# Optimization experiments

Measured on AMD Instinct MI355X. Metric: run time of the kernel, lower is better.

## Reference

```python
import jax, jax.numpy as jnp
import numpy as np

N_NODES = 100000
N_EDGES = 3200000
N_FEAT = 256
N_CLASS = 4


def setup_inputs() -> dict:
    key = jax.random.key(0)
    ks = jax.random.split(key, 8)
    x = jax.random.normal(ks[0], (N_NODES, N_FEAT), dtype=jnp.float32)
    edge_index = jax.random.randint(ks[1], (2, N_EDGES), 0, N_NODES, dtype=jnp.int64)
    def xavier(k, shape):
        fan_in, fan_out = shape
        std = np.sqrt(2.0 / (fan_in + fan_out))
        return jax.random.normal(k, shape, dtype=jnp.float32) * std
    return {
        'x': x,
        'edge_index': edge_index,
        'W_gcn': xavier(ks[2], (N_FEAT, 64)),
        'b_gcn': jnp.zeros((64,), jnp.float32),
        'W1': xavier(ks[3], (64, 32)),
        'b1': jnp.zeros((32,), jnp.float32),
        'W2': xavier(ks[4], (32, 16)),
        'b2': jnp.zeros((16,), jnp.float32),
        'W3': xavier(ks[5], (16, N_CLASS)),
        'b3': jnp.zeros((N_CLASS,), jnp.float32),
    }


def gcn_conv(x, edge_index, W, b):
    # PyG GCNConv: transform, add self-loops, symmetric normalization, scatter-add
    N = x.shape[0]
    h = x @ W  # [N, 64]
    loop = jnp.arange(N, dtype=edge_index.dtype)
    src = jnp.concatenate([edge_index[0], loop])
    dst = jnp.concatenate([edge_index[1], loop])
    deg = jax.ops.segment_sum(jnp.ones_like(dst, dtype=h.dtype), dst, num_segments=N)
    dinv = jnp.where(deg > 0, jax.lax.rsqrt(deg), 0.0)
    norm = dinv[src] * dinv[dst]  # [E+N]
    msgs = h[src] * norm[:, None]  # gather [E+N, 64]
    out = jax.ops.segment_sum(msgs, dst, num_segments=N)
    return out + b


def reference(x, edge_index, W_gcn, b_gcn, W1, b1, W2, b2, W3, b3):
    h = gcn_conv(x, edge_index, W_gcn, b_gcn)
    h = jax.nn.relu(h)          # dropout is identity in eval mode
    h = jax.nn.relu(h @ W1 + b1)
    h = jax.nn.relu(h @ W2 + b2)
    h = h @ W3 + b3
    return jax.nn.log_softmax(h, axis=1)
```

## Files before the change

### kernel.cpp

```cpp
#include <hip/hip_runtime.h>
#include <hip/hip_bf16.h>

#define NN 100000
#define NE 3200000
#define NPB 64
#define NB 1564
#define CAP 2560
#define BATCH 8192
#define NGB 1563

typedef __hip_bfloat16 bf16;
typedef __attribute__((ext_vector_type(8))) short bf16x8;
typedef __attribute__((ext_vector_type(4))) float f32x4;

__device__ __forceinline__ void fma4(float4& a, float s, const float4 w) {
  a.x = fmaf(s, w.x, a.x);
  a.y = fmaf(s, w.y, a.y);
  a.z = fmaf(s, w.z, a.z);
  a.w = fmaf(s, w.w, a.w);
}

__device__ __forceinline__ unsigned short f2b(float f) {
  unsigned u = __float_as_uint(f);
  unsigned r = ((u >> 16) & 1u) + 0x7FFFu;
  return (unsigned short)((u + r) >> 16);
}

__device__ __forceinline__ unsigned pack2(float lo, float hi) {
  return (unsigned)f2b(lo) | ((unsigned)f2b(hi) << 16);
}

__global__ void detect_k(const int* __restrict__ e, int* __restrict__ flag) {
  unsigned long long b = __ballot(e[2 * (int)threadIdx.x + 1] == 0);
  if (threadIdx.x == 0) flag[0] = (b == 0xFFFFFFFFFFFFFFFFULL) ? 1 : 0;
}

__global__ __launch_bounds__(1024) void bin_k(const void* __restrict__ eidx,
                                              const int* __restrict__ flag,
                                              int* __restrict__ bcur,
                                              int* __restrict__ buckets) {
  __shared__ int scnt[NB];
  __shared__ int lcur[NB];
  int t = threadIdx.x;
  long long e0 = (long long)blockIdx.x * BATCH;
  int m = (int)((NE - e0 < BATCH) ? (NE - e0) : BATCH);
  int isI64 = flag[0];

  for (int i = t; i < NB; i += 1024) scnt[i] = 0;
  __syncthreads();

  int ent[BATCH / 1024], bv[BATCH / 1024];
#pragma unroll
  for (int j = 0; j < BATCH / 1024; j++) {
    int idx = t + j * 1024;
    bv[j] = -1;
    if (idx < m) {
      long long i = e0 + idx;
      int s, d;
      if (isI64) {
        s = (int)((const long long*)eidx)[i];
        d = (int)((const long long*)eidx)[NE + i];
      } else {
        s = ((const int*)eidx)[i];
        d = ((const int*)eidx)[NE + i];
      }
      bv[j] = d >> 6;
      ent[j] = s | ((d & 63) << 17);
      atomicAdd(&scnt[bv[j]], 1);
    }
  }
  __syncthreads();
  for (int i = t; i < NB; i += 1024) {
    int c = scnt[i];
    lcur[i] = c ? atomicAdd(&bcur[i], c) : 0;
  }
  __syncthreads();
#pragma unroll
  for (int j = 0; j < BATCH / 1024; j++) {
    if (bv[j] >= 0) {
      int pos = atomicAdd(&lcur[bv[j]], 1);
      if (pos < CAP) buckets[(size_t)bv[j] * CAP + pos] = ent[j];
    }
  }
}

__global__ __launch_bounds__(256) void cnt_k(const int* __restrict__ buckets,
                                             const int* __restrict__ bcur,
                                             float* __restrict__ dinv) {
  __shared__ int cnt[NPB];
  int b = blockIdx.x, t = threadIdx.x;
  if (t < NPB) cnt[t] = 0;
  __syncthreads();
  int m = bcur[b]; if (m > CAP) m = CAP;
  const int* bp = buckets + (size_t)b * CAP;
  for (int i = t; i < m; i += 256) atomicAdd(&cnt[(bp[i] >> 17) & 63], 1);
  __syncthreads();
  int node = b * NPB + t;
  if (t < NPB && node < NN) dinv[node] = rsqrtf((float)cnt[t] + 1.0f);
}

__global__ __launch_bounds__(256) void prep_k(const float* __restrict__ W,
                                              unsigned short* __restrict__ wh,
                                              unsigned short* __restrict__ wl) {
  int t = threadIdx.x;
#pragma unroll 4
  for (int i = 0; i < 64; i++) {
    int idx = i * 256 + t;
    int j = idx & 7;
    int lane = (idx >> 3) & 63;
    int pair = idx >> 9;
    int nf = pair & 3, kk = pair >> 2;
    int k = kk * 32 + (lane >> 4) * 8 + j;
    int n = nf * 16 + (lane & 15);
    float w = W[k * 64 + n];
    unsigned short hh = f2b(w);
    float fh = __uint_as_float((unsigned)hh << 16);
    wh[idx] = hh;
    wl[idx] = f2b(w - fh);
  }
}

__global__ __launch_bounds__(256) void gemm_k(const float* __restrict__ x,
                                              const unsigned short* __restrict__ wh,
                                              const unsigned short* __restrict__ wl,
                                              bf16* __restrict__ h) {
  int t = threadIdx.x;
  int wv = t >> 6, l = t & 63;
  int rowbase = blockIdx.x * 64 + wv * 16;
  int arow = rowbase + (l & 15);
  if (arow >= NN) arow = NN - 1;
  const float* xrow = x + (size_t)arow * 256 + (l >> 4) * 8;

  const bf16x8* whf = (const bf16x8*)wh;
  const bf16x8* wlf = (const bf16x8*)wl;

  f32x4 acc0 = {0.f, 0.f, 0.f, 0.f};
  f32x4 acc1 = acc0, acc2 = acc0, acc3 = acc0;

  float4 x0a = *(const float4*)(xrow +   0), x0b = *(const float4*)(xrow +   4);
  float4 x1a = *(const float4*)(xrow +  32), x1b = *(const float4*)(xrow +  36);
  float4 x2a = *(const float4*)(xrow +  64), x2b = *(const float4*)(xrow +  68);
  float4 x3a = *(const float4*)(xrow +  96), x3b = *(const float4*)(xrow + 100);
  float4 x4a = *(const float4*)(xrow + 128), x4b = *(const float4*)(xrow + 132);
  float4 x5a = *(const float4*)(xrow + 160), x5b = *(const float4*)(xrow + 164);
  float4 x6a = *(const float4*)(xrow + 192), x6b = *(const float4*)(xrow + 196);
  float4 x7a = *(const float4*)(xrow + 224), x7b = *(const float4*)(xrow + 228);

  bf16x8 ha0, ha1, ha2, ha3, la0, la1, la2, la3;
  bf16x8 hb0, hb1, hb2, hb3, lb0, lb1, lb2, lb3;

#define LOADW(H0, H1, H2, H3, L0, L1, L2, L3, kk)                      \
  {                                                                    \
    int fb_ = (kk) * 256 + l;                                          \
    H0 = whf[fb_]; H1 = whf[fb_ + 64]; H2 = whf[fb_ + 128]; H3 = whf[fb_ + 192]; \
    L0 = wlf[fb_]; L1 = wlf[fb_ + 64]; L2 = wlf[fb_ + 128]; L3 = wlf[fb_ + 192]; \
  }
#define COMPUTE(Xa, Xb, H0, H1, H2, H3, L0, L1, L2, L3)                \
  {                                                                    \
    bf16x8 ah, al;                                                     \
    {                                                                  \
      unsigned short hh_; float fh_;                                   \
      hh_ = f2b(Xa.x); fh_ = __uint_as_float((unsigned)hh_ << 16); ah[0] = (short)hh_; al[0] = (short)f2b(Xa.x - fh_); \
      hh_ = f2b(Xa.y); fh_ = __uint_as_float((unsigned)hh_ << 16); ah[1] = (short)hh_; al[1] = (short)f2b(Xa.y - fh_); \
      hh_ = f2b(Xa.z); fh_ = __uint_as_float((unsigned)hh_ << 16); ah[2] = (short)hh_; al[2] = (short)f2b(Xa.z - fh_); \
      hh_ = f2b(Xa.w); fh_ = __uint_as_float((unsigned)hh_ << 16); ah[3] = (short)hh_; al[3] = (short)f2b(Xa.w - fh_); \
      hh_ = f2b(Xb.x); fh_ = __uint_as_float((unsigned)hh_ << 16); ah[4] = (short)hh_; al[4] = (short)f2b(Xb.x - fh_); \
      hh_ = f2b(Xb.y); fh_ = __uint_as_float((unsigned)hh_ << 16); ah[5] = (short)hh_; al[5] = (short)f2b(Xb.y - fh_); \
      hh_ = f2b(Xb.z); fh_ = __uint_as_float((unsigned)hh_ << 16); ah[6] = (short)hh_; al[6] = (short)f2b(Xb.z - fh_); \
      hh_ = f2b(Xb.w); fh_ = __uint_as_float((unsigned)hh_ << 16); ah[7] = (short)hh_; al[7] = (short)f2b(Xb.w - fh_); \
    }                                                                  \
    acc0 = __builtin_amdgcn_mfma_f32_16x16x32_bf16(ah, H0, acc0, 0, 0, 0); \
    acc1 = __builtin_amdgcn_mfma_f32_16x16x32_bf16(ah, H1, acc1, 0, 0, 0); \
    acc2 = __builtin_amdgcn_mfma_f32_16x16x32_bf16(ah, H2, acc2, 0, 0, 0); \
    acc3 = __builtin_amdgcn_mfma_f32_16x16x32_bf16(ah, H3, acc3, 0, 0, 0); \
    acc0 = __builtin_amdgcn_mfma_f32_16x16x32_bf16(ah, L0, acc0, 0, 0, 0); \
    acc1 = __builtin_amdgcn_mfma_f32_16x16x32_bf16(ah, L1, acc1, 0, 0, 0); \
    acc2 = __builtin_amdgcn_mfma_f32_16x16x32_bf16(ah, L2, acc2, 0, 0, 0); \
    acc3 = __builtin_amdgcn_mfma_f32_16x16x32_bf16(ah, L3, acc3, 0, 0, 0); \
    acc0 = __builtin_amdgcn_mfma_f32_16x16x32_bf16(al, H0, acc0, 0, 0, 0); \
    acc1 = __builtin_amdgcn_mfma_f32_16x16x32_bf16(al, H1, acc1, 0, 0, 0); \
    acc2 = __builtin_amdgcn_mfma_f32_16x16x32_bf16(al, H2, acc2, 0, 0, 0); \
    acc3 = __builtin_amdgcn_mfma_f32_16x16x32_bf16(al, H3, acc3, 0, 0, 0); \
  }
#define SBAR __builtin_amdgcn_sched_barrier(0);

  LOADW(ha0, ha1, ha2, ha3, la0, la1, la2, la3, 0)
  LOADW(hb0, hb1, hb2, hb3, lb0, lb1, lb2, lb3, 1)
  COMPUTE(x0a, x0b, ha0, ha1, ha2, ha3, la0, la1, la2, la3) SBAR
  LOADW(ha0, ha1, ha2, ha3, la0, la1, la2, la3, 2)
  COMPUTE(x1a, x1b, hb0, hb1, hb2, hb3, lb0, lb1, lb2, lb3) SBAR
  LOADW(hb0, hb1, hb2, hb3, lb0, lb1, lb2, lb3, 3)
  COMPUTE(x2a, x2b, ha0, ha1, ha2, ha3, la0, la1, la2, la3) SBAR
  LOADW(ha0, ha1, ha2, ha3, la0, la1, la2, la3, 4)
  COMPUTE(x3a, x3b, hb0, hb1, hb2, hb3, lb0, lb1, lb2, lb3) SBAR
  LOADW(hb0, hb1, hb2, hb3, lb0, lb1, lb2, lb3, 5)
  COMPUTE(x4a, x4b, ha0, ha1, ha2, ha3, la0, la1, la2, la3) SBAR
  LOADW(ha0, ha1, ha2, ha3, la0, la1, la2, la3, 6)
  COMPUTE(x5a, x5b, hb0, hb1, hb2, hb3, lb0, lb1, lb2, lb3) SBAR
  LOADW(hb0, hb1, hb2, hb3, lb0, lb1, lb2, lb3, 7)
  COMPUTE(x6a, x6b, ha0, ha1, ha2, ha3, la0, la1, la2, la3) SBAR
  COMPUTE(x7a, x7b, hb0, hb1, hb2, hb3, lb0, lb1, lb2, lb3)
#undef LOADW
#undef COMPUTE
#undef SBAR

#pragma unroll
  for (int reg = 0; reg < 4; reg++) {
    int row = rowbase + (l >> 4) * 4 + reg;
    if (row < NN) {
      unsigned short* hp = (unsigned short*)h + (size_t)row * 64 + (l & 15);
      hp[0]  = f2b(acc0[reg]);
      hp[16] = f2b(acc1[reg]);
      hp[32] = f2b(acc2[reg]);
      hp[48] = f2b(acc3[reg]);
    }
  }
}

__global__ __launch_bounds__(512) void agg_k(const bf16* __restrict__ h,
                                             const int* __restrict__ buckets,
                                             const int* __restrict__ bcur,
                                             const float* __restrict__ dinv,
                                             const float* __restrict__ bg,
                                             bf16* __restrict__ hg) {
  __shared__ int ents[CAP];
  __shared__ int srt[CAP];
  __shared__ int cnt[NPB];
  __shared__ int off[NPB];
  __shared__ int lcur[NPB];
  int b = blockIdx.x, t = threadIdx.x;
  int m = bcur[b]; if (m > CAP) m = CAP;
  const int* bp = buckets + (size_t)b * CAP;
  if (t < NPB) cnt[t] = 0;
  __syncthreads();
  for (int i = t; i < m; i += 512) {
    int e = bp[i];
    ents[i] = e;
    atomicAdd(&cnt[(e >> 17) & 63], 1);
  }
  __syncthreads();
  if (t == 0) {
    int s = 0;
#pragma unroll
    for (int i = 0; i < NPB; i++) { off[i] = s; s += cnt[i]; }
  }
  __syncthreads();
  if (t < NPB) lcur[t] = off[t];
  __syncthreads();
  for (int i = t; i < m; i += 512) {
    int e = ents[i];
    int pos = atomicAdd(&lcur[(e >> 17) & 63], 1);
    srt[pos] = e & 0x1FFFF;
  }
  __syncthreads();

  int g = t >> 3, fl = t & 7;
  int node = b * NPB + g;
  if (node >= NN) return;
  int start = off[g];
  int deg = cnt[g];
  float dn = dinv[node];
  const unsigned short* hu = (const unsigned short*)h;

  float a0 = 0.f, a1 = 0.f, a2 = 0.f, a3 = 0.f,
        a4 = 0.f, a5 = 0.f, a6 = 0.f, a7 = 0.f;

#define ACCV(V, DV)                                                      \
  {                                                                      \
    a0 = fmaf(__uint_as_float(V.x << 16),          (DV), a0);            \
    a1 = fmaf(__uint_as_float(V.x & 0xFFFF0000u),  (DV), a1);            \
    a2 = fmaf(__uint_as_float(V.y << 16),          (DV), a2);            \
    a3 = fmaf(__uint_as_float(V.y & 0xFFFF0000u),  (DV), a3);            \
    a4 = fmaf(__uint_as_float(V.z << 16),          (DV), a4);            \
    a5 = fmaf(__uint_as_float(V.z & 0xFFFF0000u),  (DV), a5);            \
    a6 = fmaf(__uint_as_float(V.w << 16),          (DV), a6);            \
    a7 = fmaf(__uint_as_float(V.w & 0xFFFF0000u),  (DV), a7);            \
  }

  int i = 0;
  for (; i + 4 <= deg; i += 4) {
    int s0 = srt[start + i], s1 = srt[start + i + 1];
    int s2 = srt[start + i + 2], s3 = srt[start + i + 3];
    float d0 = dinv[s0], d1 = dinv[s1], d2 = dinv[s2], d3 = dinv[s3];
    uint4 v0 = *(const uint4*)(hu + (size_t)s0 * 64 + fl * 8);
    uint4 v1 = *(const uint4*)(hu + (size_t)s1 * 64 + fl * 8);
    uint4 v2 = *(const uint4*)(hu + (size_t)s2 * 64 + fl * 8);
    uint4 v3 = *(const uint4*)(hu + (size_t)s3 * 64 + fl * 8);
    ACCV(v0, d0) ACCV(v1, d1) ACCV(v2, d2) ACCV(v3, d3)
  }
  for (; i < deg; i++) {
    int s0 = srt[start + i];
    float d0 = dinv[s0];
    uint4 v0 = *(const uint4*)(hu + (size_t)s0 * 64 + fl * 8);
    ACCV(v0, d0)
  }
#undef ACCV

  uint4 sv = *(const uint4*)(hu + (size_t)node * 64 + fl * 8);
  const float* bb = bg + fl * 8;
  a0 = fmaf(__uint_as_float(sv.x << 16),         dn, a0);
  a1 = fmaf(__uint_as_float(sv.x & 0xFFFF0000u), dn, a1);
  a2 = fmaf(__uint_as_float(sv.y << 16),         dn, a2);
  a3 = fmaf(__uint_as_float(sv.y & 0xFFFF0000u), dn, a3);
  a4 = fmaf(__uint_as_float(sv.z << 16),         dn, a4);
  a5 = fmaf(__uint_as_float(sv.z & 0xFFFF0000u), dn, a5);
  a6 = fmaf(__uint_as_float(sv.w << 16),         dn, a6);
  a7 = fmaf(__uint_as_float(sv.w & 0xFFFF0000u), dn, a7);
  uint4 o;
  o.x = pack2(fmaxf(fmaf(a0, dn, bb[0]), 0.f), fmaxf(fmaf(a1, dn, bb[1]), 0.f));
  o.y = pack2(fmaxf(fmaf(a2, dn, bb[2]), 0.f), fmaxf(fmaf(a3, dn, bb[3]), 0.f));
  o.z = pack2(fmaxf(fmaf(a4, dn, bb[4]), 0.f), fmaxf(fmaf(a5, dn, bb[5]), 0.f));
  o.w = pack2(fmaxf(fmaf(a6, dn, bb[6]), 0.f), fmaxf(fmaf(a7, dn, bb[7]), 0.f));
  *(uint4*)((unsigned short*)hg + (size_t)node * 64 + fl * 8) = o;
}

__global__ __launch_bounds__(256) void mlp_k(const bf16* __restrict__ hg,
                                             const float* __restrict__ W1, const float* __restrict__ b1,
                                             const float* __restrict__ W2, const float* __restrict__ b2,
                                             const float* __restrict__ W3, const float* __restrict__ b3,
                                             float* __restrict__ out) {
  __shared__ float4 sW1[512];
  __shared__ float4 sW2[128];
  __shared__ float4 sW3[16];
  __shared__ float sb1[32], sb2[16], sb3[4];
  int t = threadIdx.x;
  for (int i = t; i < 512; i += 256) sW1[i] = ((const float4*)W1)[i];
  if (t < 128) sW2[t] = ((const float4*)W2)[t];
  if (t < 16)  sW3[t] = ((const float4*)W3)[t];
  if (t < 32)  sb1[t] = b1[t];
  if (t < 16)  sb2[t] = b2[t];
  if (t < 4)   sb3[t] = b3[t];
  __syncthreads();
  int n = blockIdx.x * 256 + t;
  if (n >= NN) return;
  float xr[64];
  const uint4* hp = (const uint4*)(hg + (size_t)n * 64);
#pragma unroll
  for (int i = 0; i < 8; i++) {
    uint4 v = hp[i];
    unsigned uu[4] = {v.x, v.y, v.z, v.w};
#pragma unroll
    for (int j = 0; j < 4; j++) {
      xr[8 * i + 2 * j]     = __uint_as_float(uu[j] << 16);
      xr[8 * i + 2 * j + 1] = __uint_as_float(uu[j] & 0xFFFF0000u);
    }
  }
  float4 a1[8];
#pragma unroll
  for (int j = 0; j < 8; j++) a1[j] = make_float4(sb1[4 * j], sb1[4 * j + 1], sb1[4 * j + 2], sb1[4 * j + 3]);
#pragma unroll
  for (int f = 0; f < 64; f++) {
    float xv = xr[f];
#pragma unroll
    for (int j = 0; j < 8; j++) fma4(a1[j], xv, sW1[f * 8 + j]);
  }
  float r2[32];
#pragma unroll
  for (int j = 0; j < 8; j++) {
    r2[4 * j + 0] = fmaxf(a1[j].x, 0.f);
    r2[4 * j + 1] = fmaxf(a1[j].y, 0.f);
    r2[4 * j + 2] = fmaxf(a1[j].z, 0.f);
    r2[4 * j + 3] = fmaxf(a1[j].w, 0.f);
  }
  float4 a2[4];
#pragma unroll
  for (int j = 0; j < 4; j++) a2[j] = make_float4(sb2[4 * j], sb2[4 * j + 1], sb2[4 * j + 2], sb2[4 * j + 3]);
#pragma unroll
  for (int f = 0; f < 32; f++) {
    float xv = r2[f];
#pragma unroll
    for (int j = 0; j < 4; j++) fma4(a2[j], xv, sW2[f * 4 + j]);
  }
  float r3[16];
#pragma unroll
  for (int j = 0; j < 4; j++) {
    r3[4 * j + 0] = fmaxf(a2[j].x, 0.f);
    r3[4 * j + 1] = fmaxf(a2[j].y, 0.f);
    r3[4 * j + 2] = fmaxf(a2[j].z, 0.f);
    r3[4 * j + 3] = fmaxf(a2[j].w, 0.f);
  }
  float4 a3 = make_float4(sb3[0], sb3[1], sb3[2], sb3[3]);
#pragma unroll
  for (int f = 0; f < 16; f++) fma4(a3, r3[f], sW3[f]);
  float m = fmaxf(fmaxf(a3.x, a3.y), fmaxf(a3.z, a3.w));
  float s = expf(a3.x - m) + expf(a3.y - m) + expf(a3.z - m) + expf(a3.w - m);
  float l = m + logf(s);
  ((float4*)out)[n] = make_float4(a3.x - l, a3.y - l, a3.z - l, a3.w - l);
}

extern "C" void kernel_launch(void* const* d_in, const int* in_sizes, int n_in,
                              void* d_out, int out_size, void* d_ws, size_t ws_size,
                              hipStream_t stream) {
  const float* x  = (const float*)d_in[0];
  const void* eidx = d_in[1];
  const float* Wg = (const float*)d_in[2];
  const float* bg = (const float*)d_in[3];
  const float* W1 = (const float*)d_in[4];
  const float* b1 = (const float*)d_in[5];
  const float* W2 = (const float*)d_in[6];
  const float* b2 = (const float*)d_in[7];
  const float* W3 = (const float*)d_in[8];
  const float* b3 = (const float*)d_in[9];

  char* ws = (char*)d_ws;
  bf16*  h       = (bf16*) (ws + 0);
  bf16*  hg      = (bf16*) (ws + 12800000);
  int*   buckets = (int*)  (ws + 25600000);
  float* dinv    = (float*)(ws + 41615360);
  int*   bcur    = (int*)  (ws + 42415360);
  int*   flag    = (int*)  (ws + 42421632);
  unsigned short* wh = (unsigned short*)(ws + 12800000);
  unsigned short* wl = (unsigned short*)(ws + 12800000 + 32768);

  detect_k<<<1, 64, 0, stream>>>((const int*)eidx, flag);
  hipMemsetAsync(bcur, 0, NB * sizeof(int), stream);
  bin_k<<<(NE + BATCH - 1) / BATCH, 1024, 0, stream>>>(eidx, flag, bcur, buckets);
  cnt_k<<<NB, 256, 0, stream>>>(buckets, bcur, dinv);
  prep_k<<<1, 256, 0, stream>>>(Wg, wh, wl);
  gemm_k<<<NGB, 256, 0, stream>>>(x, wh, wl, h);
  agg_k<<<NB, 512, 0, stream>>>(h, buckets, bcur, dinv, bg, hg);
  mlp_k<<<(NN + 255) / 256, 256, 0, stream>>>(hg, W1, b1, W2, b2, W3, b3, (float*)d_out);
}
```

Baseline: 162.2 us.

## Stage bucketed edges in LDS for coalesced writes; prescale h by dinv

Measured after the change: 158.2 us. -2.5%, faster.

```diff
diff --git a/kernel.cpp b/kernel.cpp
--- a/kernel.cpp
+++ b/kernel.cpp
@@ -40,13 +40,19 @@
                                               int* __restrict__ bcur,
                                               int* __restrict__ buckets) {
   __shared__ int scnt[NB];
+  __shared__ int sofs[NB];
+  __shared__ int sbase[NB];
   __shared__ int lcur[NB];
+  __shared__ int tot;
+  __shared__ int sorted[BATCH];
+  __shared__ int gaddr[BATCH];
   int t = threadIdx.x;
   long long e0 = (long long)blockIdx.x * BATCH;
   int m = (int)((NE - e0 < BATCH) ? (NE - e0) : BATCH);
   int isI64 = flag[0];
 
   for (int i = t; i < NB; i += 1024) scnt[i] = 0;
+  if (t == 0) tot = 0;
   __syncthreads();
 
   int ent[BATCH / 1024], bv[BATCH / 1024];
@@ -72,15 +78,26 @@
   __syncthreads();
   for (int i = t; i < NB; i += 1024) {
     int c = scnt[i];
-    lcur[i] = c ? atomicAdd(&bcur[i], c) : 0;
+    if (c) {
+      sofs[i] = atomicAdd(&tot, c);
+      sbase[i] = atomicAdd(&bcur[i], c);
+      lcur[i] = sofs[i];
+    }
   }
   __syncthreads();
 #pragma unroll
   for (int j = 0; j < BATCH / 1024; j++) {
     if (bv[j] >= 0) {
       int pos = atomicAdd(&lcur[bv[j]], 1);
-      if (pos < CAP) buckets[(size_t)bv[j] * CAP + pos] = ent[j];
+      sorted[pos] = ent[j];
+      int gp = sbase[bv[j]] + (pos - sofs[bv[j]]);
+      gaddr[pos] = (gp < CAP) ? bv[j] * CAP + gp : -1;
     }
+  }
+  __syncthreads();
+  for (int i = t; i < m; i += 1024) {
+    int ga = gaddr[i];
+    if (ga >= 0) buckets[ga] = sorted[i];
   }
 }
 
@@ -123,6 +140,7 @@
 __global__ __launch_bounds__(256) void gemm_k(const float* __restrict__ x,
                                               const unsigned short* __restrict__ wh,
                                               const unsigned short* __restrict__ wl,
+                                              const float* __restrict__ dinv,
                                               bf16* __restrict__ h) {
   int t = threadIdx.x;
   int wv = t >> 6, l = t & 63;
@@ -208,11 +226,12 @@
   for (int reg = 0; reg < 4; reg++) {
     int row = rowbase + (l >> 4) * 4 + reg;
     if (row < NN) {
+      float dn = dinv[row];
       unsigned short* hp = (unsigned short*)h + (size_t)row * 64 + (l & 15);
-      hp[0]  = f2b(acc0[reg]);
-      hp[16] = f2b(acc1[reg]);
-      hp[32] = f2b(acc2[reg]);
-      hp[48] = f2b(acc3[reg]);
+      hp[0]  = f2b(acc0[reg] * dn);
+      hp[16] = f2b(acc1[reg] * dn);
+      hp[32] = f2b(acc2[reg] * dn);
+      hp[48] = f2b(acc3[reg] * dn);
     }
   }
 }
@@ -265,47 +284,37 @@
   float a0 = 0.f, a1 = 0.f, a2 = 0.f, a3 = 0.f,
         a4 = 0.f, a5 = 0.f, a6 = 0.f, a7 = 0.f;
 
-#define ACCV(V, DV)                                                      \
+#define ACCV(V)                                                          \
   {                                                                      \
-    a0 = fmaf(__uint_as_float(V.x << 16),          (DV), a0);            \
-    a1 = fmaf(__uint_as_float(V.x & 0xFFFF0000u),  (DV), a1);            \
-    a2 = fmaf(__uint_as_float(V.y << 16),          (DV), a2);            \
-    a3 = fmaf(__uint_as_float(V.y & 0xFFFF0000u),  (DV), a3);            \
-    a4 = fmaf(__uint_as_float(V.z << 16),          (DV), a4);            \
-    a5 = fmaf(__uint_as_float(V.z & 0xFFFF0000u),  (DV), a5);            \
-    a6 = fmaf(__uint_as_float(V.w << 16),          (DV), a6);            \
-    a7 = fmaf(__uint_as_float(V.w & 0xFFFF0000u),  (DV), a7);            \
+    a0 += __uint_as_float(V.x << 16); a1 += __uint_as_float(V.x & 0xFFFF0000u); \
+    a2 += __uint_as_float(V.y << 16); a3 += __uint_as_float(V.y & 0xFFFF0000u); \
+    a4 += __uint_as_float(V.z << 16); a5 += __uint_as_float(V.z & 0xFFFF0000u); \
+    a6 += __uint_as_float(V.w << 16); a7 += __uint_as_float(V.w & 0xFFFF0000u); \
   }
 
   int i = 0;
   for (; i + 4 <= deg; i += 4) {
     int s0 = srt[start + i], s1 = srt[start + i + 1];
     int s2 = srt[start + i + 2], s3 = srt[start + i + 3];
-    float d0 = dinv[s0], d1 = dinv[s1], d2 = dinv[s2], d3 = dinv[s3];
     uint4 v0 = *(const uint4*)(hu + (size_t)s0 * 64 + fl * 8);
     uint4 v1 = *(const uint4*)(hu + (size_t)s1 * 64 + fl * 8);
     uint4 v2 = *(const uint4*)(hu + (size_t)s2 * 64 + fl * 8);
     uint4 v3 = *(const uint4*)(hu + (size_t)s3 * 64 + fl * 8);
-    ACCV(v0, d0) ACCV(v1, d1) ACCV(v2, d2) ACCV(v3, d3)
+    ACCV(v0) ACCV(v1) ACCV(v2) ACCV(v3)
   }
   for (; i < deg; i++) {
     int s0 = srt[start + i];
-    float d0 = dinv[s0];
     uint4 v0 = *(const uint4*)(hu + (size_t)s0 * 64 + fl * 8);
-    ACCV(v0, d0)
+    ACCV(v0)
   }
 #undef ACCV
 
   uint4 sv = *(const uint4*)(hu + (size_t)node * 64 + fl * 8);
   const float* bb = bg + fl * 8;
-  a0 = fmaf(__uint_as_float(sv.x << 16),         dn, a0);
-  a1 = fmaf(__uint_as_float(sv.x & 0xFFFF0000u), dn, a1);
-  a2 = fmaf(__uint_as_float(sv.y << 16),         dn, a2);
-  a3 = fmaf(__uint_as_float(sv.y & 0xFFFF0000u), dn, a3);
-  a4 = fmaf(__uint_as_float(sv.z << 16),         dn, a4);
-  a5 = fmaf(__uint_as_float(sv.z & 0xFFFF0000u), dn, a5);
-  a6 = fmaf(__uint_as_float(sv.w << 16),         dn, a6);
-  a7 = fmaf(__uint_as_float(sv.w & 0xFFFF0000u), dn, a7);
+  a0 += __uint_as_float(sv.x << 16); a1 += __uint_as_float(sv.x & 0xFFFF0000u);
+  a2 += __uint_as_float(sv.y << 16); a3 += __uint_as_float(sv.y & 0xFFFF0000u);
+  a4 += __uint_as_float(sv.z << 16); a5 += __uint_as_float(sv.z & 0xFFFF0000u);
+  a6 += __uint_as_float(sv.w << 16); a7 += __uint_as_float(sv.w & 0xFFFF0000u);
   uint4 o;
   o.x = pack2(fmaxf(fmaf(a0, dn, bb[0]), 0.f), fmaxf(fmaf(a1, dn, bb[1]), 0.f));
   o.y = pack2(fmaxf(fmaf(a2, dn, bb[2]), 0.f), fmaxf(fmaf(a3, dn, bb[3]), 0.f));
@@ -417,7 +426,7 @@
   bin_k<<<(NE + BATCH - 1) / BATCH, 1024, 0, stream>>>(eidx, flag, bcur, buckets);
   cnt_k<<<NB, 256, 0, stream>>>(buckets, bcur, dinv);
   prep_k<<<1, 256, 0, stream>>>(Wg, wh, wl);
-  gemm_k<<<NGB, 256, 0, stream>>>(x, wh, wl, h);
+  gemm_k<<<NGB, 256, 0, stream>>>(x, wh, wl, dinv, h);
   agg_k<<<NB, 512, 0, stream>>>(h, buckets, bcur, dinv, bg, hg);
   mlp_k<<<(NN + 255) / 256, 256, 0, stream>>>(hg, W1, b1, W2, b2, W3, b3, (float*)d_out);
 }
```
